# Optimization experiments

Hardware: AMD Instinct MI355X
Metric: run time of the kernel (lower is better)

## Reference

```python
import jax, jax.numpy as jnp
import numpy as np

E = 64  # embedding_size
N_NODES = 100000
N_FACTS = 100000  # ground facts per relation
ARITY_GROUPS = {1: 2, 2: 3, 3: 2, 4: 1}  # arity -> number of relations with that arity


def mish(x):
    return x * jnp.tanh(jax.nn.softplus(x))


def _group_messages(node_embeddings, idx, wi, bi, wo, bo, arity):
    # idx: [G, F*arity] flat node indices for G relations of this arity
    G, L = idx.shape
    x = node_embeddings[idx]                      # [G, F*arity, E] gather
    x = x.reshape(G, L // arity, arity * E)       # [G, F, arity*E]
    h = mish(jnp.einsum('gfi,goi->gfo', x, wi) + bi[:, None, :])
    y = jnp.einsum('gfi,goi->gfo', h, wo) + bo[:, None, :]
    msgs = (x + y).reshape(-1, E)                 # residual, back to [G*F*arity, E]
    return msgs, idx.reshape(-1)


def setup_inputs():
    key = jax.random.key(0)
    ks = jax.random.split(key, 16)
    inp = {"node_embeddings": jax.random.normal(ks[0], (N_NODES, E), jnp.float32)}
    k = 1
    for a, G in ARITY_GROUPS.items():
        d = a * E
        inp[f"idx_a{a}"] = jax.random.randint(ks[k], (G, N_FACTS * a), 0, N_NODES); k += 1
        inp[f"wi_a{a}"] = jax.random.normal(ks[k], (G, d, d), jnp.float32) / np.sqrt(d).astype(np.float32); k += 1
        inp[f"bi_a{a}"] = jnp.zeros((G, d), jnp.float32)
        inp[f"wo_a{a}"] = jax.random.normal(ks[k], (G, d, d), jnp.float32) / np.sqrt(d).astype(np.float32); k += 1
        inp[f"bo_a{a}"] = jnp.zeros((G, d), jnp.float32)
    return inp


def reference(node_embeddings,
              idx_a1, wi_a1, bi_a1, wo_a1, bo_a1,
              idx_a2, wi_a2, bi_a2, wo_a2, bo_a2,
              idx_a3, wi_a3, bi_a3, wo_a3, bo_a3,
              idx_a4, wi_a4, bi_a4, wo_a4, bo_a4):
    groups = [
        (idx_a1, wi_a1, bi_a1, wo_a1, bo_a1, 1),
        (idx_a2, wi_a2, bi_a2, wo_a2, bo_a2, 2),
        (idx_a3, wi_a3, bi_a3, wo_a3, bo_a3, 3),
        (idx_a4, wi_a4, bi_a4, wo_a4, bo_a4, 4),
    ]
    msgs_list, idx_list = [], []
    for idx, wi, bi, wo, bo, a in groups:  # fixed small loop over arity groups
        m, i = _group_messages(node_embeddings, idx, wi, bi, wo, bo, a)
        msgs_list.append(m)
        idx_list.append(i)
    output_messages = jnp.concatenate(msgs_list, axis=0)   # [sum G*F*a, E]
    output_indices = jnp.concatenate(idx_list, axis=0)
    return output_messages, output_indices
```

## Files before the change

kernel.cpp:

```cpp
#include <hip/hip_runtime.h>
#include <hip/hip_bf16.h>

#define NF 100000
#define TM 64
#define NB 1563

typedef __attribute__((ext_vector_type(8))) short bf16x8;
typedef __attribute__((ext_vector_type(4))) short bf16x4;
typedef __attribute__((ext_vector_type(4))) float f32x4;

__device__ __forceinline__ short bfs(float x) {
    union { __hip_bfloat16 h; short s; } u;
    u.h = __float2bfloat16(x);
    return u.s;
}

__device__ __forceinline__ float b2f(short s) {
    union { float f; unsigned u; } u;
    u.u = ((unsigned)(unsigned short)s) << 16;
    return u.f;
}

__device__ __forceinline__ bf16x8 cvt8(const float4 a, const float4 b) {
    bf16x8 r;
    r[0] = bfs(a.x); r[1] = bfs(a.y); r[2] = bfs(a.z); r[3] = bfs(a.w);
    r[4] = bfs(b.x); r[5] = bfs(b.y); r[6] = bfs(b.z); r[7] = bfs(b.w);
    return r;
}

__device__ __forceinline__ float mish_f(float v) {
    float t = __expf(v);
    float p = t * (t + 2.0f);
    float r = v * p * __builtin_amdgcn_rcpf(p + 2.0f);
    return (v > 20.0f) ? v : r;
}

struct CvtA {
    const float* src[8];
    long pre[9];
    int  Dv[8];
    const float* emb;
    long embElems;
};

__global__ __launch_bounds__(256)
void cvt_all(CvtA a, __hip_bfloat16* __restrict__ dst) {
    long e = ((long)blockIdx.x * 256 + threadIdx.x) * 8;
    if (e < a.embElems) {
        const float4* s = (const float4*)(a.emb + e);
        *(bf16x8*)(dst + e) = cvt8(s[0], s[1]);
        return;
    }
    long we = e - a.embElems;
    if (we >= a.pre[8]) return;
    int j = 0;
    #pragma unroll
    for (int q = 0; q < 8; q++) if (we >= a.pre[q + 1]) j = q + 1;
    long le = we - a.pre[j];
    const int D = a.Dv[j];
    int g = (int)(le / ((long)D * D));
    int rem = (int)(le - (long)g * D * D);
    int n = rem / D;
    int k = rem - n * D;
    const float4* s = (const float4*)(a.src[j] + le);
    long off = a.embElems + a.pre[j] + (long)g * D * D + (long)(k >> 5) * 32 * D + n * 32 + (k & 31);
    *(bf16x8*)(dst + off) = cvt8(s[0], s[1]);
}

template<int D, int A, int WMODE>
__device__ __forceinline__ void body(
    int fb, int g,
    const __hip_bfloat16* __restrict__ emb, const int* __restrict__ idx,
    const __hip_bfloat16* __restrict__ wi, const float* __restrict__ bi,
    const __hip_bfloat16* __restrict__ wo, const float* __restrict__ bo,
    float* __restrict__ out_msgs, float* __restrict__ out_idx,
    __hip_bfloat16* __restrict__ buf)
{
    constexpr int DP = D + 8;
    constexpr int CT = D / 64;
    constexpr int KS = D / 32;
    constexpr int RC = D / 8;
    constexpr int CH = (TM * RC) / 256;

    const int f0   = fb * TM;
    const int tid  = threadIdx.x;
    const int lane = tid & 63;
    const int w    = tid >> 6;
    const long gFA = (long)g * NF * A;
    const int valid = min(TM, NF - f0);
    const int* idx_g = idx + gFA + (long)f0 * A;

    const int ar = lane & 15;
    const int kg = lane >> 4;
    const int c0 = w * (D / 4);
    const long wlane = (long)g * D * D + (long)(c0 + ar) * 32 + kg * 8;

    __hip_bfloat16* X = buf;
    __hip_bfloat16* H = (WMODE == 0) ? buf + TM * DP : buf;

    {
        int nodes[CH];
        #pragma unroll
        for (int j = 0; j < CH; j++) {
            int c = tid + j * 256;
            int r = c / RC;
            nodes[j] = (r < valid) ? idx_g[r * A + ((c % RC) >> 3)] : idx_g[0];
        }
        bf16x8 v[CH];
        #pragma unroll
        for (int j = 0; j < CH; j++) {
            int c = tid + j * 256;
            v[j] = *(const bf16x8*)(emb + (long)nodes[j] * 64 + (((c % RC) * 8) & 63));
        }
        #pragma unroll
        for (int j = 0; j < CH; j++) {
            int c = tid + j * 256;
            *(bf16x8*)(X + (c / RC) * DP + (c % RC) * 8) = v[j];
        }
        if (tid < valid * A)
            __builtin_nontemporal_store((float)idx_g[tid], &out_idx[gFA + (long)f0 * A + tid]);
    }

    f32x4 acc[4][CT];
    #pragma unroll
    for (int rt = 0; rt < 4; rt++)
        #pragma unroll
        for (int ct = 0; ct < CT; ct++) acc[rt][ct] = (f32x4)0.0f;

    if constexpr (WMODE == 0) {
        bf16x8 wia[KS][CT];
        #pragma unroll
        for (int ks = 0; ks < KS; ks++)
            #pragma unroll
            for (int ct = 0; ct < CT; ct++)
                wia[ks][ct] = *(const bf16x8*)(wi + wlane + (long)ks * 32 * D + ct * 512);

        __syncthreads();

        #pragma unroll
        for (int ks = 0; ks < KS; ks++) {
            const int kk = ks * 32;
            bf16x8 xb[4];
            #pragma unroll
            for (int rt = 0; rt < 4; rt++)
                xb[rt] = *(const bf16x8*)(X + (rt * 16 + ar) * DP + kk + kg * 8);
            __builtin_amdgcn_s_setprio(1);
            #pragma unroll
            for (int ct = 0; ct < CT; ct++)
                #pragma unroll
                for (int rt = 0; rt < 4; rt++)
                    acc[rt][ct] = __builtin_amdgcn_mfma_f32_16x16x32_bf16(wia[ks][ct], xb[rt], acc[rt][ct], 0, 0, 0);
            __builtin_amdgcn_s_setprio(0);
        }

        bf16x8 woa[KS][CT];
        #pragma unroll
        for (int ks = 0; ks < KS; ks++)
            #pragma unroll
            for (int ct = 0; ct < CT; ct++)
                woa[ks][ct] = *(const bf16x8*)(wo + wlane + (long)ks * 32 * D + ct * 512);

        #pragma unroll
        for (int ct = 0; ct < CT; ct++) {
            const int cb = c0 + ct * 16 + kg * 4;
            const float4 bi4 = *(const float4*)(bi + g * D + cb);
            #pragma unroll
            for (int rt = 0; rt < 4; rt++) {
                bf16x4 hv;
                hv[0] = bfs(mish_f(acc[rt][ct][0] + bi4.x));
                hv[1] = bfs(mish_f(acc[rt][ct][1] + bi4.y));
                hv[2] = bfs(mish_f(acc[rt][ct][2] + bi4.z));
                hv[3] = bfs(mish_f(acc[rt][ct][3] + bi4.w));
                *(bf16x4*)(H + (rt * 16 + ar) * DP + cb) = hv;
            }
        }
        __syncthreads();

        #pragma unroll
        for (int rt = 0; rt < 4; rt++)
            #pragma unroll
            for (int ct = 0; ct < CT; ct++) acc[rt][ct] = (f32x4)0.0f;

        #pragma unroll
        for (int ks = 0; ks < KS; ks++) {
            const int kk = ks * 32;
            bf16x8 hb[4];
            #pragma unroll
            for (int rt = 0; rt < 4; rt++)
                hb[rt] = *(const bf16x8*)(H + (rt * 16 + ar) * DP + kk + kg * 8);
            __builtin_amdgcn_s_setprio(1);
            #pragma unroll
            for (int ct = 0; ct < CT; ct++)
                #pragma unroll
                for (int rt = 0; rt < 4; rt++)
                    acc[rt][ct] = __builtin_amdgcn_mfma_f32_16x16x32_bf16(woa[ks][ct], hb[rt], acc[rt][ct], 0, 0, 0);
            __builtin_amdgcn_s_setprio(0);
        }

        float* ob = out_msgs + (gFA + (long)f0 * A) * 64;
        #pragma unroll
        for (int ct = 0; ct < CT; ct++) {
            const int cb = c0 + ct * 16 + kg * 4;
            const float4 bo4 = *(const float4*)(bo + g * D + cb);
            #pragma unroll
            for (int rt = 0; rt < 4; rt++) {
                const int r = rt * 16 + ar;
                bf16x4 xv = *(const bf16x4*)(X + (rt * 16 + ar) * DP + cb);
                f32x4 o;
                o[0] = acc[rt][ct][0] + bo4.x + b2f(xv[0]);
                o[1] = acc[rt][ct][1] + bo4.y + b2f(xv[1]);
                o[2] = acc[rt][ct][2] + bo4.z + b2f(xv[2]);
                o[3] = acc[rt][ct][3] + bo4.w + b2f(xv[3]);
                if (r < valid)
                    __builtin_nontemporal_store(o, (f32x4*)(ob + (long)r * D + cb));
            }
        }
    } else {
        bf16x8 wcur[CT];
        if constexpr (WMODE == 1) {
            #pragma unroll
            for (int ct = 0; ct < CT; ct++)
                wcur[ct] = *(const bf16x8*)(wi + wlane + ct * 512);
        }
        __syncthreads();

        #pragma unroll
        for (int ks = 0; ks < KS; ks++) {
            const int kk = ks * 32;
            bf16x8 xb[4];
            #pragma unroll
            for (int rt = 0; rt < 4; rt++)
                xb[rt] = *(const bf16x8*)(X + (rt * 16 + ar) * DP + kk + kg * 8);
            if constexpr (WMODE == 1) {
                bf16x8 wnx[CT];
                if (ks + 1 < KS)
                    #pragma unroll
                    for (int ct = 0; ct < CT; ct++)
                        wnx[ct] = *(const bf16x8*)(wi + wlane + (long)(ks + 1) * 32 * D + ct * 512);
                __builtin_amdgcn_s_setprio(1);
                #pragma unroll
                for (int ct = 0; ct < CT; ct++)
                    #pragma unroll
                    for (int rt = 0; rt < 4; rt++)
                        acc[rt][ct] = __builtin_amdgcn_mfma_f32_16x16x32_bf16(wcur[ct], xb[rt], acc[rt][ct], 0, 0, 0);
                __builtin_amdgcn_s_setprio(0);
                if (ks + 1 < KS)
                    #pragma unroll
                    for (int ct = 0; ct < CT; ct++) wcur[ct] = wnx[ct];
            } else {
                bf16x8 wf[CT];
                #pragma unroll
                for (int ct = 0; ct < CT; ct++)
                    wf[ct] = *(const bf16x8*)(wi + wlane + (long)ks * 32 * D + ct * 512);
                __builtin_amdgcn_s_setprio(1);
                #pragma unroll
                for (int ct = 0; ct < CT; ct++)
                    #pragma unroll
                    for (int rt = 0; rt < 4; rt++)
                        acc[rt][ct] = __builtin_amdgcn_mfma_f32_16x16x32_bf16(wf[ct], xb[rt], acc[rt][ct], 0, 0, 0);
                __builtin_amdgcn_s_setprio(0);
            }
        }

        __syncthreads();

        #pragma unroll
        for (int ct = 0; ct < CT; ct++) {
            const int cb = c0 + ct * 16 + kg * 4;
            const float4 bi4 = *(const float4*)(bi + g * D + cb);
            #pragma unroll
            for (int rt = 0; rt < 4; rt++) {
                bf16x4 hv;
                hv[0] = bfs(mish_f(acc[rt][ct][0] + bi4.x));
                hv[1] = bfs(mish_f(acc[rt][ct][1] + bi4.y));
                hv[2] = bfs(mish_f(acc[rt][ct][2] + bi4.z));
                hv[3] = bfs(mish_f(acc[rt][ct][3] + bi4.w));
                *(bf16x4*)(H + (rt * 16 + ar) * DP + cb) = hv;
            }
        }
        __syncthreads();

        #pragma unroll
        for (int rt = 0; rt < 4; rt++)
            #pragma unroll
            for (int ct = 0; ct < CT; ct++) acc[rt][ct] = (f32x4)0.0f;

        if constexpr (WMODE == 1) {
            #pragma unroll
            for (int ct = 0; ct < CT; ct++)
                wcur[ct] = *(const bf16x8*)(wo + wlane + ct * 512);
        }

        #pragma unroll
        for (int ks = 0; ks < KS; ks++) {
            const int kk = ks * 32;
            bf16x8 hb[4];
            #pragma unroll
            for (int rt = 0; rt < 4; rt++)
                hb[rt] = *(const bf16x8*)(H + (rt * 16 + ar) * DP + kk + kg * 8);
            if constexpr (WMODE == 1) {
                bf16x8 wnx[CT];
                if (ks + 1 < KS)
                    #pragma unroll
                    for (int ct = 0; ct < CT; ct++)
                        wnx[ct] = *(const bf16x8*)(wo + wlane + (long)(ks + 1) * 32 * D + ct * 512);
                __builtin_amdgcn_s_setprio(1);
                #pragma unroll
                for (int ct = 0; ct < CT; ct++)
                    #pragma unroll
                    for (int rt = 0; rt < 4; rt++)
                        acc[rt][ct] = __builtin_amdgcn_mfma_f32_16x16x32_bf16(wcur[ct], hb[rt], acc[rt][ct], 0, 0, 0);
                __builtin_amdgcn_s_setprio(0);
                if (ks + 1 < KS)
                    #pragma unroll
                    for (int ct = 0; ct < CT; ct++) wcur[ct] = wnx[ct];
            } else {
                bf16x8 wf[CT];
                #pragma unroll
                for (int ct = 0; ct < CT; ct++)
                    wf[ct] = *(const bf16x8*)(wo + wlane + (long)ks * 32 * D + ct * 512);
                __builtin_amdgcn_s_setprio(1);
                #pragma unroll
                for (int ct = 0; ct < CT; ct++)
                    #pragma unroll
                    for (int rt = 0; rt < 4; rt++)
                        acc[rt][ct] = __builtin_amdgcn_mfma_f32_16x16x32_bf16(wf[ct], hb[rt], acc[rt][ct], 0, 0, 0);
                __builtin_amdgcn_s_setprio(0);
            }
        }

        float* ob = out_msgs + (gFA + (long)f0 * A) * 64;
        #pragma unroll
        for (int ct = 0; ct < CT; ct++) {
            const int cb = c0 + ct * 16 + kg * 4;
            const int sres = (c0 + ct * 16) >> 6;
            const float4 bo4 = *(const float4*)(bo + g * D + cb);
            #pragma unroll
            for (int rt = 0; rt < 4; rt++) {
                const int r = rt * 16 + ar;
                int node = idx_g[min(r, valid - 1) * A + sres];
                bf16x4 xv = *(const bf16x4*)(emb + (long)node * 64 + (cb & 63));
                f32x4 o;
                o[0] = acc[rt][ct][0] + bo4.x + b2f(xv[0]);
                o[1] = acc[rt][ct][1] + bo4.y + b2f(xv[1]);
                o[2] = acc[rt][ct][2] + bo4.z + b2f(xv[2]);
                o[3] = acc[rt][ct][3] + bo4.w + b2f(xv[3]);
                if (r < valid)
                    __builtin_nontemporal_store(o, (f32x4*)(ob + (long)r * D + cb));
            }
        }
    }
}

struct KArgs {
    const __hip_bfloat16* emb;
    const int* idx[4];
    const __hip_bfloat16* wi[4]; const float* bi[4];
    const __hip_bfloat16* wo[4]; const float* bo[4];
    float* om[4]; float* oi[4];
};

__global__ __launch_bounds__(256, 4)
void fused_kernel(KArgs a) {
    __shared__ __hip_bfloat16 buf[2 * TM * 136];
    const int b = blockIdx.x;
    if (b < NB) {
        body<256, 4, 2>(b, 0, a.emb, a.idx[3], a.wi[3], a.bi[3], a.wo[3], a.bo[3], a.om[3], a.oi[3], buf);
    } else if (b < NB * 3) {
        int r = b - NB;
        body<192, 3, 1>(r % NB, r / NB, a.emb, a.idx[2], a.wi[2], a.bi[2], a.wo[2], a.bo[2], a.om[2], a.oi[2], buf);
    } else if (b < NB * 6) {
        int r = b - NB * 3;
        body<128, 2, 0>(r % NB, r / NB, a.emb, a.idx[1], a.wi[1], a.bi[1], a.wo[1], a.bo[1], a.om[1], a.oi[1], buf);
    } else {
        int r = b - NB * 6;
        body<64, 1, 0>(r % NB, r / NB, a.emb, a.idx[0], a.wi[0], a.bi[0], a.wo[0], a.bo[0], a.om[0], a.oi[0], buf);
    }
}

template<int D, int A, int MINW>
__global__ __launch_bounds__(256, MINW)
void msg_kernel(const float* __restrict__ embv,
                const int* __restrict__ idx,
                const float* __restrict__ wiv, const float* __restrict__ bi,
                const float* __restrict__ wov, const float* __restrict__ bo,
                float* __restrict__ out_msgs, float* __restrict__ out_idx)
{
    constexpr int DP = D + 8;
    constexpr int CT = D / 64;
    constexpr int KS = D / 32;
    constexpr int RC = D / 8;
    __shared__ __hip_bfloat16 buf[TM][DP];

    const int g    = blockIdx.y;
    const int f0   = blockIdx.x * TM;
    const int tid  = threadIdx.x;
    const int lane = tid & 63;
    const int w    = tid >> 6;
    const long gFA = (long)g * NF * A;
    const int valid = min(TM, NF - f0);

    {
        const int* idx_g = idx + gFA + (long)f0 * A;
        #pragma unroll
        for (int c = tid; c < TM * RC; c += 256) {
            int r = c / RC;
            int i = (c - r * RC) * 8;
            bf16x8 v = (bf16x8)0;
            if (r < valid) {
                int node = idx_g[r * A + (i >> 6)];
                const float4* s = (const float4*)(embv + (long)node * 64 + (i & 63));
                v = cvt8(s[0], s[1]);
            }
            *(bf16x8*)(&buf[r][i]) = v;
        }
        if (tid < valid * A) out_idx[gFA + (long)f0 * A + tid] = (float)idx_g[tid];
    }
    __syncthreads();

    const int ar = lane & 15;
    const int kg = lane >> 4;
    const int c0 = w * (D / 4);
    const long wbase = (long)g * D * D;

    f32x4 acc[4][CT];
    #pragma unroll
    for (int rt = 0; rt < 4; rt++)
        #pragma unroll
        for (int ct = 0; ct < CT; ct++) acc[rt][ct] = (f32x4)0.0f;

    #pragma unroll
    for (int ks = 0; ks < KS; ks++) {
        const int kk = ks * 32;
        bf16x8 xb[4];
        #pragma unroll
        for (int rt = 0; rt < 4; rt++) xb[rt] = *(const bf16x8*)(&buf[rt * 16 + ar][kk + kg * 8]);
        #pragma unroll
        for (int ct = 0; ct < CT; ct++) {
            const float4* bp = (const float4*)(wiv + wbase + (long)(c0 + ct * 16 + ar) * D + kk + kg * 8);
            bf16x8 wf = cvt8(bp[0], bp[1]);
            #pragma unroll
            for (int rt = 0; rt < 4; rt++)
                acc[rt][ct] = __builtin_amdgcn_mfma_f32_16x16x32_bf16(wf, xb[rt], acc[rt][ct], 0, 0, 0);
        }
    }

    bf16x4 res[4][CT];
    #pragma unroll
    for (int ct = 0; ct < CT; ct++) {
        const int cb = c0 + ct * 16 + kg * 4;
        #pragma unroll
        for (int rt = 0; rt < 4; rt++)
            res[rt][ct] = *(const bf16x4*)(&buf[rt * 16 + ar][cb]);
    }
    __syncthreads();

    #pragma unroll
    for (int ct = 0; ct < CT; ct++) {
        const int cb = c0 + ct * 16 + kg * 4;
        const float4 bi4 = *(const float4*)(bi + g * D + cb);
        #pragma unroll
        for (int rt = 0; rt < 4; rt++) {
            bf16x4 hv;
            hv[0] = bfs(mish_f(acc[rt][ct][0] + bi4.x));
            hv[1] = bfs(mish_f(acc[rt][ct][1] + bi4.y));
            hv[2] = bfs(mish_f(acc[rt][ct][2] + bi4.z));
            hv[3] = bfs(mish_f(acc[rt][ct][3] + bi4.w));
            *(bf16x4*)(&buf[rt * 16 + ar][cb]) = hv;
        }
    }
    __syncthreads();

    #pragma unroll
    for (int rt = 0; rt < 4; rt++)
        #pragma unroll
        for (int ct = 0; ct < CT; ct++) acc[rt][ct] = (f32x4)0.0f;

    #pragma unroll
    for (int ks = 0; ks < KS; ks++) {
        const int kk = ks * 32;
        bf16x8 hb[4];
        #pragma unroll
        for (int rt = 0; rt < 4; rt++) hb[rt] = *(const bf16x8*)(&buf[rt * 16 + ar][kk + kg * 8]);
        #pragma unroll
        for (int ct = 0; ct < CT; ct++) {
            const float4* bp = (const float4*)(wov + wbase + (long)(c0 + ct * 16 + ar) * D + kk + kg * 8);
            bf16x8 wf = cvt8(bp[0], bp[1]);
            #pragma unroll
            for (int rt = 0; rt < 4; rt++)
                acc[rt][ct] = __builtin_amdgcn_mfma_f32_16x16x32_bf16(wf, hb[rt], acc[rt][ct], 0, 0, 0);
        }
    }

    {
        float* ob = out_msgs + (gFA + (long)f0 * A) * 64;
        #pragma unroll
        for (int ct = 0; ct < CT; ct++) {
            const int cb = c0 + ct * 16 + kg * 4;
            const float4 bo4 = *(const float4*)(bo + g * D + cb);
            #pragma unroll
            for (int rt = 0; rt < 4; rt++) {
                const int r = rt * 16 + ar;
                float4 o;
                o.x = acc[rt][ct][0] + bo4.x + b2f(res[rt][ct][0]);
                o.y = acc[rt][ct][1] + bo4.y + b2f(res[rt][ct][1]);
                o.z = acc[rt][ct][2] + bo4.z + b2f(res[rt][ct][2]);
                o.w = acc[rt][ct][3] + bo4.w + b2f(res[rt][ct][3]);
                if (r < valid) *(float4*)(ob + (long)r * D + cb) = o;
            }
        }
    }
}

extern "C" void kernel_launch(void* const* d_in, const int* in_sizes, int n_in,
                              void* d_out, int out_size, void* d_ws, size_t ws_size,
                              hipStream_t stream) {
    const float* emb_f = (const float*)d_in[0];
    const int Gs[4] = {2, 3, 2, 1};
    const int Ds[4] = {64, 128, 192, 256};

    const int*   idx_a[4];
    const float *wi_f[4], *bi_f[4], *wo_f[4], *bo_f[4];
    for (int k = 0; k < 4; k++) {
        idx_a[k] = (const int*)d_in[1 + 5 * k];
        wi_f[k]  = (const float*)d_in[2 + 5 * k];
        bi_f[k]  = (const float*)d_in[3 + 5 * k];
        wo_f[k]  = (const float*)d_in[4 + 5 * k];
        bo_f[k]  = (const float*)d_in[5 + 5 * k];
    }

    float* out = (float*)d_out;
    const long MSG_ELEMS = 115200000L;
    const long rowOff[4] = {0, 200000, 800000, 1400000};
    float* om[4]; float* oi[4];
    for (int k = 0; k < 4; k++) {
        om[k] = out + rowOff[k] * 64;
        oi[k] = out + MSG_ELEMS + rowOff[k];
    }

    const long EMB_ELEMS = 6400000L;
    long wPre[9]; wPre[0] = 0;
    int  wD[8];
    for (int k = 0; k < 4; k++) {
        long we = (long)Gs[k] * Ds[k] * Ds[k];
        wPre[2 * k + 1] = wPre[2 * k] + we;
        wPre[2 * k + 2] = wPre[2 * k + 1] + we;
        wD[2 * k] = Ds[k]; wD[2 * k + 1] = Ds[k];
    }
    const long NEED = (EMB_ELEMS + wPre[8]) * 2;

    if (ws_size >= (size_t)NEED) {
        __hip_bfloat16* emb_b = (__hip_bfloat16*)d_ws;
        __hip_bfloat16* w_b   = emb_b + EMB_ELEMS;

        CvtA ca;
        for (int k = 0; k < 4; k++) { ca.src[2 * k] = wi_f[k]; ca.src[2 * k + 1] = wo_f[k]; }
        for (int j = 0; j < 9; j++) ca.pre[j] = wPre[j];
        for (int j = 0; j < 8; j++) ca.Dv[j] = wD[j];
        ca.emb = emb_f;
        ca.embElems = EMB_ELEMS;
        long totChunks = (EMB_ELEMS + wPre[8]) / 8;
        cvt_all<<<dim3((totChunks + 255) / 256), dim3(256), 0, stream>>>(ca, emb_b);

        KArgs a;
        a.emb = emb_b;
        for (int k = 0; k < 4; k++) {
            a.idx[k] = idx_a[k];
            a.wi[k] = w_b + wPre[2 * k];
            a.wo[k] = w_b + wPre[2 * k + 1];
            a.bi[k] = bi_f[k];
            a.bo[k] = bo_f[k];
            a.om[k] = om[k];
            a.oi[k] = oi[k];
        }
        fused_kernel<<<dim3(NB * 8), dim3(256), 0, stream>>>(a);
    } else {
        msg_kernel<64, 1, 4><<<dim3(NB, 2), 256, 0, stream>>>(
            emb_f, idx_a[0], wi_f[0], bi_f[0], wo_f[0], bo_f[0], om[0], oi[0]);
        msg_kernel<128, 2, 4><<<dim3(NB, 3), 256, 0, stream>>>(
            emb_f, idx_a[1], wi_f[1], bi_f[1], wo_f[1], bo_f[1], om[1], oi[1]);
        msg_kernel<192, 3, 4><<<dim3(NB, 2), 256, 0, stream>>>(
            emb_f, idx_a[2], wi_f[2], bi_f[2], wo_f[2], bo_f[2], om[2], oi[2]);
        msg_kernel<256, 4, 3><<<dim3(NB, 1), 256, 0, stream>>>(
            emb_f, idx_a[3], wi_f[3], bi_f[3], wo_f[3], bo_f[3], om[3], oi[3]);
    }
}
```

Measured before the change: 198.9 us.

## Gather embeddings directly into LDS with XOR-swizzled layout instead of padding

Replaces the register-staged embedding gather with global_load_lds direct-to-LDS 16-byte loads, and swaps the padded row layout (D+8) for an XOR swizzle on 8-element chunks to avoid bank conflicts. All LDS reads and writes of X and H go through the swizzle helper, and the shared buffer shrinks to TM*256. This removes VGPR pressure and the extra LDS store pass during the gather, and the smaller LDS footprint may allow more resident blocks. It risks missing waits: the direct-to-LDS loads rely on the existing barrier to drain vmcnt before X is read.

```diff
diff --git a/kernel.cpp b/kernel.cpp
--- a/kernel.cpp
+++ b/kernel.cpp
@@ -33,6 +33,12 @@
     float p = t * (t + 2.0f);
     float r = v * p * __builtin_amdgcn_rcpf(p + 2.0f);
     return (v > 20.0f) ? v : r;
+}
+
+__device__ __forceinline__ void gld16(const __hip_bfloat16* g, __hip_bfloat16* l) {
+    __builtin_amdgcn_global_load_lds(
+        (const __attribute__((address_space(1))) void*)g,
+        (__attribute__((address_space(3))) void*)l, 16, 0, 0);
 }
 
 struct CvtA {
@@ -76,7 +82,6 @@
     float* __restrict__ out_msgs, float* __restrict__ out_idx,
     __hip_bfloat16* __restrict__ buf)
 {
-    constexpr int DP = D + 8;
     constexpr int CT = D / 64;
     constexpr int KS = D / 32;
     constexpr int RC = D / 8;
@@ -96,26 +101,20 @@
     const long wlane = (long)g * D * D + (long)(c0 + ar) * 32 + kg * 8;
 
     __hip_bfloat16* X = buf;
-    __hip_bfloat16* H = (WMODE == 0) ? buf + TM * DP : buf;
+    __hip_bfloat16* H = (WMODE == 0) ? buf + TM * D : buf;
+
+    auto sx = [&](__hip_bfloat16* base, int r, int e) -> __hip_bfloat16* {
+        return base + (r * RC + (((e >> 3)) ^ (r & 7))) * 8 + (e & 7);
+    };
 
     {
-        int nodes[CH];
-        #pragma unroll
-        for (int j = 0; j < CH; j++) {
-            int c = tid + j * 256;
+        #pragma unroll
+        for (int q = 0; q < CH; q++) {
+            int c = tid + q * 256;
             int r = c / RC;
-            nodes[j] = (r < valid) ? idx_g[r * A + ((c % RC) >> 3)] : idx_g[0];
-        }
-        bf16x8 v[CH];
-        #pragma unroll
-        for (int j = 0; j < CH; j++) {
-            int c = tid + j * 256;
-            v[j] = *(const bf16x8*)(emb + (long)nodes[j] * 64 + (((c % RC) * 8) & 63));
-        }
-        #pragma unroll
-        for (int j = 0; j < CH; j++) {
-            int c = tid + j * 256;
-            *(bf16x8*)(X + (c / RC) * DP + (c % RC) * 8) = v[j];
+            int jg = (c % RC) ^ (r & 7);
+            int node = idx_g[min(r, valid - 1) * A + (jg >> 3)];
+            gld16(emb + (long)node * 64 + (jg & 7) * 8, X + c * 8);
         }
         if (tid < valid * A)
             __builtin_nontemporal_store((float)idx_g[tid], &out_idx[gFA + (long)f0 * A + tid]);
@@ -143,7 +142,7 @@
             bf16x8 xb[4];
             #pragma unroll
             for (int rt = 0; rt < 4; rt++)
-                xb[rt] = *(const bf16x8*)(X + (rt * 16 + ar) * DP + kk + kg * 8);
+                xb[rt] = *(const bf16x8*)sx(X, rt * 16 + ar, kk + kg * 8);
             __builtin_amdgcn_s_setprio(1);
             #pragma unroll
             for (int ct = 0; ct < CT; ct++)
@@ -171,7 +170,7 @@
                 hv[1] = bfs(mish_f(acc[rt][ct][1] + bi4.y));
                 hv[2] = bfs(mish_f(acc[rt][ct][2] + bi4.z));
                 hv[3] = bfs(mish_f(acc[rt][ct][3] + bi4.w));
-                *(bf16x4*)(H + (rt * 16 + ar) * DP + cb) = hv;
+                *(bf16x4*)sx(H, rt * 16 + ar, cb) = hv;
             }
         }
         __syncthreads();
@@ -187,7 +186,7 @@
             bf16x8 hb[4];
             #pragma unroll
             for (int rt = 0; rt < 4; rt++)
-                hb[rt] = *(const bf16x8*)(H + (rt * 16 + ar) * DP + kk + kg * 8);
+                hb[rt] = *(const bf16x8*)sx(H, rt * 16 + ar, kk + kg * 8);
             __builtin_amdgcn_s_setprio(1);
             #pragma unroll
             for (int ct = 0; ct < CT; ct++)
@@ -205,7 +204,7 @@
             #pragma unroll
             for (int rt = 0; rt < 4; rt++) {
                 const int r = rt * 16 + ar;
-                bf16x4 xv = *(const bf16x4*)(X + (rt * 16 + ar) * DP + cb);
+                bf16x4 xv = *(const bf16x4*)sx(X, r, cb);
                 f32x4 o;
                 o[0] = acc[rt][ct][0] + bo4.x + b2f(xv[0]);
                 o[1] = acc[rt][ct][1] + bo4.y + b2f(xv[1]);
@@ -230,7 +229,7 @@
             bf16x8 xb[4];
             #pragma unroll
             for (int rt = 0; rt < 4; rt++)
-                xb[rt] = *(const bf16x8*)(X + (rt * 16 + ar) * DP + kk + kg * 8);
+                xb[rt] = *(const bf16x8*)sx(X, rt * 16 + ar, kk + kg * 8);
             if constexpr (WMODE == 1) {
                 bf16x8 wnx[CT];
                 if (ks + 1 < KS)
@@ -275,7 +274,7 @@
                 hv[1] = bfs(mish_f(acc[rt][ct][1] + bi4.y));
                 hv[2] = bfs(mish_f(acc[rt][ct][2] + bi4.z));
                 hv[3] = bfs(mish_f(acc[rt][ct][3] + bi4.w));
-                *(bf16x4*)(H + (rt * 16 + ar) * DP + cb) = hv;
+                *(bf16x4*)sx(H, rt * 16 + ar, cb) = hv;
             }
         }
         __syncthreads();
@@ -297,7 +296,7 @@
             bf16x8 hb[4];
             #pragma unroll
             for (int rt = 0; rt < 4; rt++)
-                hb[rt] = *(const bf16x8*)(H + (rt * 16 + ar) * DP + kk + kg * 8);
+                hb[rt] = *(const bf16x8*)sx(H, rt * 16 + ar, kk + kg * 8);
             if constexpr (WMODE == 1) {
                 bf16x8 wnx[CT];
                 if (ks + 1 < KS)
@@ -362,7 +361,7 @@
 
 __global__ __launch_bounds__(256, 4)
 void fused_kernel(KArgs a) {
-    __shared__ __hip_bfloat16 buf[2 * TM * 136];
+    __shared__ __hip_bfloat16 buf[TM * 256];
     const int b = blockIdx.x;
     if (b < NB) {
         body<256, 4, 2>(b, 0, a.emb, a.idx[3], a.wi[3], a.bi[3], a.wo[3], a.bo[3], a.om[3], a.oi[3], buf);
```

New measurement: 202.1 us. Within noise of the previous version (+1.6%).
